# Kernel optimization log

Measured on AMD Instinct MI355X. Metric: run time of the kernel, lower is better.

Reference implementation:

```python
import jax, jax.numpy as jnp
import numpy as np

B, N, D = 8, 1024, 384
L, NH = 2, 8
HD = D // NH
HID2 = 4 * D  # project_in output channels = 2 * hidden = 2 * (2*dim) = 1536
HID = 2 * D  # GDFN hidden = 768


def setup_inputs() -> dict:
    key = jax.random.key(0)
    ks = jax.random.split(key, 16)
    s = 0.02
    return {
        "x": jax.random.normal(ks[0], (B, N, D), jnp.float32),
        "qkv_w": jax.random.normal(ks[1], (L, 3 * D, D), jnp.float32) * s,
        "qkv_b": jnp.zeros((L, 3 * D), jnp.float32),
        "proj_w": jax.random.normal(ks[2], (L, D, D), jnp.float32) * s,
        "proj_b": jnp.zeros((L, D), jnp.float32),
        "ln1_g": jnp.ones((L, D), jnp.float32),
        "ln1_b": jnp.zeros((L, D), jnp.float32),
        "ln2_g": jnp.ones((L, D), jnp.float32),
        "ln2_b": jnp.zeros((L, D), jnp.float32),
        "pin_w": jax.random.normal(ks[3], (L, HID2, D), jnp.float32) * s,
        "pin_b": jnp.zeros((L, HID2), jnp.float32),
        "dw_w": jax.random.normal(ks[4], (L, HID2, 1, 3, 3), jnp.float32) * s,
        "dw_b": jnp.zeros((L, HID2), jnp.float32),
        "pout_w": jax.random.normal(ks[5], (L, D, HID), jnp.float32) * s,
        "pout_b": jnp.zeros((L, D), jnp.float32),
    }


def _ln(y, g, b, eps=1e-5):
    m = y.mean(-1, keepdims=True)
    v = ((y - m) ** 2).mean(-1, keepdims=True)
    return (y - m) / jnp.sqrt(v + eps) * g + b


def _decay_bias(n, num_heads):
    # bias[h,i,j] = |i-j| * log(1 - 2^(-2 - 4*h/num_heads))  (negative)
    h = jnp.arange(num_heads, dtype=jnp.float32)
    decay = jnp.log(1.0 - 2.0 ** (-2.0 - 4.0 * h / num_heads))
    idx = jnp.arange(n, dtype=jnp.float32)
    dist = jnp.abs(idx[:, None] - idx[None, :])
    return dist[None] * decay[:, None, None]  # [NH, N, N]


def reference(x, qkv_w, qkv_b, proj_w, proj_b, ln1_g, ln1_b, ln2_g, ln2_b,
              pin_w, pin_b, dw_w, dw_b, pout_w, pout_b):
    b, n, d = x.shape
    hs = ws = int(np.sqrt(n))
    bias = _decay_bias(n, NH).astype(x.dtype)
    scale = HD ** -0.5
    nl = qkv_w.shape[0]
    for l in range(nl):
        # --- MHSA with spectral decay bias ---
        res = x
        xn = _ln(x, ln1_g[l], ln1_b[l])
        qkv = xn @ qkv_w[l].T + qkv_b[l]
        q, k, v = jnp.split(qkv, 3, axis=-1)
        q = q.reshape(b, n, NH, HD).transpose(0, 2, 1, 3)  # bhnd
        k = k.reshape(b, n, NH, HD).transpose(0, 2, 1, 3)
        v = v.reshape(b, n, NH, HD).transpose(0, 2, 1, 3)
        scores = jnp.einsum('bhnd,bhmd->bhnm', q, k) * scale + bias[None]
        attn = jax.nn.softmax(scores, axis=-1)
        out = jnp.einsum('bhnm,bhmd->bhnd', attn, v)
        out = out.transpose(0, 2, 1, 3).reshape(b, n, d)
        x = res + out @ proj_w[l].T + proj_b[l]
        # --- GDFN ---
        res = x
        xn = _ln(x, ln2_g[l], ln2_b[l])
        img = xn.transpose(0, 2, 1).reshape(b, d, hs, ws)  # NCHW
        h = jnp.einsum('oc,bchw->bohw', pin_w[l], img) + pin_b[l][None, :, None, None]
        h = jax.lax.conv_general_dilated(
            h, dw_w[l], window_strides=(1, 1), padding=[(1, 1), (1, 1)],
            feature_group_count=h.shape[1],
            dimension_numbers=('NCHW', 'OIHW', 'NCHW')) + dw_b[l][None, :, None, None]
        h1, h2 = jnp.split(h, 2, axis=1)
        g = jax.nn.gelu(h1, approximate=False) * h2
        o = jnp.einsum('oc,bchw->bohw', pout_w[l], g) + pout_b[l][None, :, None, None]
        x = res + o.reshape(b, d, n).transpose(0, 2, 1)
    return x
```

## Files before the change

kernel.cpp:

```cpp
#include <hip/hip_runtime.h>
#include <math.h>

#define B_ 8
#define N_ 1024
#define D_ 384
#define NH_ 8
#define HD_ 48
#define HID2_ 1536
#define HID_ 768
#define M_ (B_*N_)

typedef __attribute__((ext_vector_type(4))) float f32x4;
typedef __attribute__((ext_vector_type(2))) float f32x2;
typedef __attribute__((ext_vector_type(8))) short bf16x8;
typedef __attribute__((ext_vector_type(4))) short bf16x4;
typedef __attribute__((ext_vector_type(2))) unsigned u32x2;
typedef __attribute__((ext_vector_type(4))) unsigned u32x4;

__device__ inline unsigned short f2bf(float f) {
    unsigned u = __builtin_bit_cast(unsigned, f);
    u += 0x7fff + ((u >> 16) & 1);
    return (unsigned short)(u >> 16);
}
__device__ inline float bf2f(unsigned short h) {
    unsigned u = ((unsigned)h) << 16;
    return __builtin_bit_cast(float, u);
}
__device__ inline unsigned cvtpk_bf16(float lo, float hi) {
    unsigned r;
    asm("v_cvt_pk_bf16_f32 %0, %1, %2" : "=v"(r) : "v"(lo), "v"(hi));
    return r;
}
__device__ inline f32x4 mfma16(bf16x4 a, bf16x4 b, f32x4 c) {
#if __has_builtin(__builtin_amdgcn_mfma_f32_16x16x16bf16_1k)
    return __builtin_amdgcn_mfma_f32_16x16x16bf16_1k(a, b, c, 0, 0, 0);
#else
    asm("v_mfma_f32_16x16x16_bf16 %0, %1, %2, %0" : "+v"(c) : "v"(a), "v"(b));
    return c;
#endif
}

__global__ __launch_bounds__(256) void cvt4_kernel(
    const float* __restrict__ s1, const float* __restrict__ s2,
    const float* __restrict__ s3, const float* __restrict__ s4,
    int c1, int c2, int c3, int c4, unsigned short* __restrict__ out) {
    int i = blockIdx.x * 256 + threadIdx.x;
    if (i >= c1 + c2 + c3 + c4) return;
    const float* src; int off = i;
    if (i < c1) { src = s1; }
    else if (i < c1 + c2) { src = s2; off = i - c1; }
    else if (i < c1 + c2 + c3) { src = s3; off = i - c1 - c2; }
    else { src = s4; off = i - c1 - c2 - c3; }
    f32x4 v = *(const f32x4*)(src + (size_t)off*4);
    ushort4 o;
    o.x = f2bf(v[0]); o.y = f2bf(v[1]); o.z = f2bf(v[2]); o.w = f2bf(v[3]);
    *(ushort4*)(out + (size_t)i*4) = o;
}

__global__ __launch_bounds__(256) void ln_kernel(
    const float* __restrict__ x, const float* __restrict__ g,
    const float* __restrict__ b, unsigned short* __restrict__ out) {
    int wave = threadIdx.x >> 6;
    int lane = threadIdx.x & 63;
    int row  = blockIdx.x * 4 + wave;
    const float* xr = x + (size_t)row * D_;
    f32x2 v[3];
    float s = 0.f;
    #pragma unroll
    for (int i = 0; i < 3; ++i) {
        v[i] = *(const f32x2*)(xr + i*128 + lane*2);
        s += v[i][0] + v[i][1];
    }
    #pragma unroll
    for (int off = 1; off < 64; off <<= 1) s += __shfl_xor(s, off);
    float mean = s * (1.0f/D_);
    float vs = 0.f;
    #pragma unroll
    for (int i = 0; i < 3; ++i) {
        float t0 = v[i][0]-mean, t1 = v[i][1]-mean;
        vs += t0*t0 + t1*t1;
    }
    #pragma unroll
    for (int off = 1; off < 64; off <<= 1) vs += __shfl_xor(vs, off);
    float rstd = rsqrtf(vs * (1.0f/D_) + 1e-5f);
    unsigned short* orow = out + (size_t)row * D_;
    #pragma unroll
    for (int i = 0; i < 3; ++i) {
        int d = i*128 + lane*2;
        ushort2 o;
        o.x = f2bf((v[i][0]-mean)*rstd*g[d]   + b[d]);
        o.y = f2bf((v[i][1]-mean)*rstd*g[d+1] + b[d+1]);
        *(ushort2*)(orow + d) = o;
    }
}

template<int MODE>
__global__ __launch_bounds__(256) void gemm_bf16(
    const unsigned short* __restrict__ A, const unsigned short* __restrict__ W,
    const float* __restrict__ bias, const float* __restrict__ res,
    void* __restrict__ outv, int M, int O, int K) {
    __shared__ unsigned short a_s[128][40];
    __shared__ unsigned short w_s[128][40];
    int tid = threadIdx.x;
    int o0 = blockIdx.x * 128;
    int m0 = blockIdx.y * 128;
    int wave = tid >> 6, lane = tid & 63;
    int wm = wave >> 1, wn = wave & 1;
    int lr = lane & 15, lc = lane >> 4;
    int r0 = tid >> 2, ch = tid & 3;
    int r1 = r0 + 64;
    f32x4 acc[4][4];
    #pragma unroll
    for (int i=0;i<4;++i)
      #pragma unroll
      for (int j=0;j<4;++j) acc[i][j] = (f32x4){0.f,0.f,0.f,0.f};

    const unsigned short* pa0 = A + (size_t)(m0+r0)*K + ch*8;
    const unsigned short* pa1 = A + (size_t)(m0+r1)*K + ch*8;
    const unsigned short* pw0 = W + (size_t)(o0+r0)*K + ch*8;
    const unsigned short* pw1 = W + (size_t)(o0+r1)*K + ch*8;
    bf16x8 a0 = *(const bf16x8*)pa0, a1 = *(const bf16x8*)pa1;
    bf16x8 w0 = *(const bf16x8*)pw0, w1 = *(const bf16x8*)pw1;

    for (int k0 = 0; k0 < K; k0 += 32) {
        __syncthreads();
        *(bf16x8*)&a_s[r0][ch*8] = a0;
        *(bf16x8*)&a_s[r1][ch*8] = a1;
        *(bf16x8*)&w_s[r0][ch*8] = w0;
        *(bf16x8*)&w_s[r1][ch*8] = w1;
        __syncthreads();
        if (k0 + 32 < K) {
            pa0 += 32; pa1 += 32; pw0 += 32; pw1 += 32;
            a0 = *(const bf16x8*)pa0; a1 = *(const bf16x8*)pa1;
            w0 = *(const bf16x8*)pw0; w1 = *(const bf16x8*)pw1;
        }
        bf16x8 af[4], wf[4];
        #pragma unroll
        for (int i = 0; i < 4; ++i)
            af[i] = *(const bf16x8*)&a_s[wm*64 + i*16 + lr][lc*8];
        #pragma unroll
        for (int j = 0; j < 4; ++j)
            wf[j] = *(const bf16x8*)&w_s[wn*64 + j*16 + lr][lc*8];
        #pragma unroll
        for (int i = 0; i < 4; ++i)
            #pragma unroll
            for (int j = 0; j < 4; ++j)
                acc[i][j] = __builtin_amdgcn_mfma_f32_16x16x32_bf16(
                    af[i], wf[j], acc[i][j], 0, 0, 0);
    }
    #pragma unroll
    for (int i = 0; i < 4; ++i) {
        int mbase = m0 + wm*64 + i*16 + lc*4;
        #pragma unroll
        for (int j = 0; j < 4; ++j) {
            int oc = o0 + wn*64 + j*16 + lr;
            float bv = bias[oc];
            #pragma unroll
            for (int r = 0; r < 4; ++r) {
                int m = mbase + r;
                float v = acc[i][j][r] + bv;
                if (MODE == 1) {
                    ((float*)outv)[(size_t)m*O + oc] = v + res[(size_t)m*O + oc];
                } else {
                    ((unsigned short*)outv)[(size_t)m*O + oc] = f2bf(v);
                }
            }
        }
    }
}

template<int MODE>
__global__ __launch_bounds__(256) void gemm_bf16_s(
    const unsigned short* __restrict__ A, const unsigned short* __restrict__ W,
    const float* __restrict__ bias, const float* __restrict__ res,
    void* __restrict__ outv, int M, int O, int K) {
    __shared__ unsigned short a_s[64][72];
    __shared__ unsigned short w_s[64][72];
    int tid = threadIdx.x;
    int o0 = blockIdx.x * 64;
    int m0 = blockIdx.y * 64;
    int wave = tid >> 6, lane = tid & 63;
    int lr = lane & 15, lc = lane >> 4;
    int r = tid >> 2, c = (tid & 3) * 16;
    f32x4 acc[4];
    #pragma unroll
    for (int i=0;i<4;++i) acc[i] = (f32x4){0.f,0.f,0.f,0.f};

    const unsigned short* pa = A + (size_t)(m0+r)*K + c;
    const unsigned short* pw = W + (size_t)(o0+r)*K + c;
    bf16x8 a0 = *(const bf16x8*)pa, a1 = *(const bf16x8*)(pa+8);
    bf16x8 w0 = *(const bf16x8*)pw, w1 = *(const bf16x8*)(pw+8);

    for (int k0 = 0; k0 < K; k0 += 64) {
        __syncthreads();
        *(bf16x8*)&a_s[r][c]   = a0;
        *(bf16x8*)&a_s[r][c+8] = a1;
        *(bf16x8*)&w_s[r][c]   = w0;
        *(bf16x8*)&w_s[r][c+8] = w1;
        __syncthreads();
        if (k0 + 64 < K) {
            pa += 64; pw += 64;
            a0 = *(const bf16x8*)pa; a1 = *(const bf16x8*)(pa+8);
            w0 = *(const bf16x8*)pw; w1 = *(const bf16x8*)(pw+8);
        }
        #pragma unroll
        for (int ks = 0; ks < 2; ++ks) {
            bf16x8 wf = *(const bf16x8*)&w_s[wave*16 + lr][ks*32 + lc*8];
            #pragma unroll
            for (int i = 0; i < 4; ++i) {
                bf16x8 af = *(const bf16x8*)&a_s[i*16 + lr][ks*32 + lc*8];
                acc[i] = __builtin_amdgcn_mfma_f32_16x16x32_bf16(af, wf, acc[i], 0,0,0);
            }
        }
    }
    int oc = o0 + wave*16 + lr;
    float bv = bias[oc];
    #pragma unroll
    for (int i = 0; i < 4; ++i) {
        #pragma unroll
        for (int rr = 0; rr < 4; ++rr) {
            int m = m0 + i*16 + lc*4 + rr;
            float v = acc[i][rr] + bv;
            if (MODE == 1) {
                ((float*)outv)[(size_t)m*O + oc] = v + res[(size_t)m*O + oc];
            } else {
                ((unsigned short*)outv)[(size_t)m*O + oc] = f2bf(v);
            }
        }
    }
}

__global__ __launch_bounds__(256) void attn_mfma(
    const unsigned short* __restrict__ qkv, unsigned short* __restrict__ out) {
    __shared__ unsigned short k_s[64][72];
    __shared__ unsigned short vt_s[48][72];
    int tid = threadIdx.x;
    int wave = tid >> 6, lane = tid & 63;
    int lr = lane & 15, lc = lane >> 4;
    int b = blockIdx.x >> 3, h = blockIdx.x & 7;
    int q0 = blockIdx.y * 64;
    const float LOG2E = 1.4426950408889634f;
    float decay_nats = logf(1.0f - exp2f(-2.0f - 0.5f*(float)h));
    float decay = decay_nats * LOG2E;
    const float scale2 = 0.14433756729740643f * LOG2E;
    const bf16x8 zero8 = {0,0,0,0,0,0,0,0};

    int bandi = (int)(20.0f / (-decay_nats));
    int lo = q0 - bandi - 63;
    int kt_lo = lo > 0 ? (lo >> 6) : 0;
    int kt_hi = (q0 + 63 + bandi) >> 6;
    if (kt_hi > 15) kt_hi = 15;

    if (tid < 192) {
        int zr = tid / 3, zc = 48 + (tid % 3) * 8;
        *(bf16x8*)&k_s[zr][zc] = zero8;
    }

    int q = q0 + wave*16 + lr;
    float qqf = (float)q;
    const unsigned short* qrow = qkv + ((size_t)b*N_ + q)*1152 + h*48;
    bf16x8 qf0 = *(const bf16x8*)(qrow + lc*8);
    bf16x8 qf1 = zero8;
    if (lc < 2) qf1 = *(const bf16x8*)(qrow + 32 + lc*8);

    const unsigned short* kbase = qkv + (size_t)b*N_*1152 + D_ + h*48;
    int kr0 = tid / 6, kc0 = (tid % 6) * 8;
    bool kact1 = tid < 128;
    int s1 = kact1 ? tid + 256 : 0;
    int kr1 = s1 / 6, kc1 = (s1 % 6) * 8;
    const unsigned short* kp0 = kbase + (size_t)(kt_lo*64 + kr0)*1152 + kc0;
    const unsigned short* kp1 = kbase + (size_t)(kt_lo*64 + kr1)*1152 + kc1;

    int vd2 = (tid >> 3) * 2;
    int vch = tid & 7;
    bool vact = tid < 192;
    const unsigned short* vp = kbase + D_ + (size_t)(kt_lo*64 + vch*8)*1152 + vd2;

    float m_i = -3e38f, l_i = 0.f;
    f32x4 oacc[3];
    #pragma unroll
    for (int i=0;i<3;++i) oacc[i] = (f32x4){0.f,0.f,0.f,0.f};

    for (int kt = kt_lo; kt <= kt_hi; ++kt) {
        int n0 = kt * 64;
        bf16x8 kv0 = *(const bf16x8*)kp0;  kp0 += 64*1152;
        bf16x8 kv1 = zero8;
        if (kact1) kv1 = *(const bf16x8*)kp1;
        kp1 += 64*1152;
        unsigned vv[8];
        if (vact) {
            #pragma unroll
            for (int i = 0; i < 8; ++i)
                vv[i] = *(const unsigned*)(vp + (size_t)i*1152);
        }
        vp += 64*1152;
        __syncthreads();
        *(bf16x8*)&k_s[kr0][kc0] = kv0;
        if (kact1) *(bf16x8*)&k_s[kr1][kc1] = kv1;
        if (vact) {
            u32x4 wlo, whi;
            #pragma unroll
            for (int i = 0; i < 4; ++i) {
                wlo[i] = (vv[2*i] & 0xffffu) | (vv[2*i+1] << 16);
                whi[i] = (vv[2*i] >> 16)    | (vv[2*i+1] & 0xffff0000u);
            }
            *(bf16x8*)&vt_s[vd2]  [vch*8] = __builtin_bit_cast(bf16x8, wlo);
            *(bf16x8*)&vt_s[vd2+1][vch*8] = __builtin_bit_cast(bf16x8, whi);
        }
        __syncthreads();
        f32x4 sc[4];
        #pragma unroll
        for (int f = 0; f < 4; ++f) {
            sc[f] = (f32x4){0.f,0.f,0.f,0.f};
            bf16x8 kf0 = *(const bf16x8*)&k_s[f*16 + lr][lc*8];
            bf16x8 kf1 = *(const bf16x8*)&k_s[f*16 + lr][32 + lc*8];
            sc[f] = __builtin_amdgcn_mfma_f32_16x16x32_bf16(kf0, qf0, sc[f],0,0,0);
            sc[f] = __builtin_amdgcn_mfma_f32_16x16x32_bf16(kf1, qf1, sc[f],0,0,0);
        }
        float s2[4][4];
        float kv0f = (float)(n0 + lc*4);
        float mt = -3e38f;
        #pragma unroll
        for (int f = 0; f < 4; ++f)
            #pragma unroll
            for (int r = 0; r < 4; ++r) {
                float kk = kv0f + (float)(f*16 + r);
                s2[f][r] = sc[f][r]*scale2 + fabsf(qqf - kk)*decay;
                mt = fmaxf(mt, s2[f][r]);
            }
        mt = fmaxf(mt, __shfl_xor(mt, 16));
        mt = fmaxf(mt, __shfl_xor(mt, 32));
        float mn = fmaxf(m_i, mt);
        float alpha = __builtin_amdgcn_exp2f(m_i - mn);
        m_i = mn;
        l_i *= alpha;
        #pragma unroll
        for (int md = 0; md < 3; ++md)
            #pragma unroll
            for (int r = 0; r < 4; ++r) oacc[md][r] *= alpha;
        float ps = 0.f;
        #pragma unroll
        for (int f = 0; f < 4; ++f)
            #pragma unroll
            for (int r = 0; r < 4; ++r) {
                s2[f][r] = __builtin_amdgcn_exp2f(s2[f][r] - m_i);
                ps += s2[f][r];
            }
        ps += __shfl_xor(ps, 16);
        ps += __shfl_xor(ps, 32);
        l_i += ps;
        bf16x4 pfrag[4];
        #pragma unroll
        for (int f = 0; f < 4; ++f) {
            u32x2 u;
            u[0] = cvtpk_bf16(s2[f][0], s2[f][1]);
            u[1] = cvtpk_bf16(s2[f][2], s2[f][3]);
            pfrag[f] = __builtin_bit_cast(bf16x4, u);
        }
        #pragma unroll
        for (int f = 0; f < 4; ++f)
            #pragma unroll
            for (int md = 0; md < 3; ++md) {
                bf16x4 va = *(const bf16x4*)&vt_s[md*16 + lr][f*16 + lc*4];
                oacc[md] = mfma16(va, pfrag[f], oacc[md]);
            }
    }
    float inv_l = 1.0f / l_i;
    #pragma unroll
    for (int md = 0; md < 3; ++md) {
        ushort4 o;
        o.x = f2bf(oacc[md][0]*inv_l);
        o.y = f2bf(oacc[md][1]*inv_l);
        o.z = f2bf(oacc[md][2]*inv_l);
        o.w = f2bf(oacc[md][3]*inv_l);
        *(ushort4*)(out + ((size_t)b*N_ + q)*D_ + h*48 + md*16 + lc*4) = o;
    }
}

__global__ __launch_bounds__(256) void dwconv_gate_bf16(
    const unsigned short* __restrict__ h, const float* __restrict__ dw_w,
    const float* __restrict__ dw_b, unsigned short* __restrict__ g) {
    __shared__ float wt_s[9][128];
    __shared__ float bs_s[128];
    int tid = threadIdx.x;
    int cg0 = blockIdx.x * 64;
    int y   = blockIdx.y;
    int b   = blockIdx.z;
    for (int i = tid; i < 1152; i += 256) {
        int tap = i >> 7, cl = i & 127;
        int gch = (cl < 64) ? (cg0 + cl) : (HID_ + cg0 + (cl - 64));
        wt_s[tap][cl] = dw_w[(size_t)gch*9 + tap];
    }
    if (tid < 128) {
        int gch = (tid < 64) ? (cg0 + tid) : (HID_ + cg0 + (tid - 64));
        bs_s[tid] = dw_b[gch];
    }
    __syncthreads();
    int x  = tid >> 3;
    int co = (tid & 7) * 8;
    int c1 = cg0 + co;
    const unsigned short* hb = h + (size_t)b*N_*HID2_;
    float acc1[8], acc2[8];
    #pragma unroll
    for (int j=0;j<8;++j) { acc1[j] = bs_s[co+j]; acc2[j] = bs_s[64+co+j]; }
    #pragma unroll
    for (int ky=0; ky<3; ++ky) {
        int yy = y + ky - 1;
        if (yy < 0 || yy >= 32) continue;
        #pragma unroll
        for (int kx=0; kx<3; ++kx) {
            int xx = x + kx - 1;
            if (xx < 0 || xx >= 32) continue;
            const unsigned short* p = hb + (size_t)(yy*32+xx)*HID2_ + c1;
            bf16x8 d1 = *(const bf16x8*)p;
            bf16x8 d2 = *(const bf16x8*)(p + HID_);
            int t = ky*3 + kx;
            f32x4 w1a = *(const f32x4*)&wt_s[t][co];
            f32x4 w1b = *(const f32x4*)&wt_s[t][co+4];
            f32x4 w2a = *(const f32x4*)&wt_s[t][64+co];
            f32x4 w2b = *(const f32x4*)&wt_s[t][64+co+4];
            #pragma unroll
            for (int j=0;j<4;++j) {
                acc1[j]   += bf2f((unsigned short)d1[j])   * w1a[j];
                acc1[j+4] += bf2f((unsigned short)d1[j+4]) * w1b[j];
                acc2[j]   += bf2f((unsigned short)d2[j])   * w2a[j];
                acc2[j+4] += bf2f((unsigned short)d2[j+4]) * w2b[j];
            }
        }
    }
    bf16x8 o;
    #pragma unroll
    for (int j=0;j<8;++j) {
        float ge = 0.5f*acc1[j]*(1.0f + erff(acc1[j]*0.70710678118f));
        o[j] = (short)f2bf(ge * acc2[j]);
    }
    *(bf16x8*)(g + (size_t)(b*N_ + y*32 + x)*HID_ + c1) = o;
}

extern "C" void kernel_launch(void* const* d_in, const int* in_sizes, int n_in,
                              void* d_out, int out_size, void* d_ws, size_t ws_size,
                              hipStream_t stream) {
    const float* x_in   = (const float*)d_in[0];
    const float* qkv_w  = (const float*)d_in[1];
    const float* qkv_b  = (const float*)d_in[2];
    const float* proj_w = (const float*)d_in[3];
    const float* proj_b = (const float*)d_in[4];
    const float* ln1_g  = (const float*)d_in[5];
    const float* ln1_b  = (const float*)d_in[6];
    const float* ln2_g  = (const float*)d_in[7];
    const float* ln2_b  = (const float*)d_in[8];
    const float* pin_w  = (const float*)d_in[9];
    const float* pin_b  = (const float*)d_in[10];
    const float* dw_w   = (const float*)d_in[11];
    const float* dw_b   = (const float*)d_in[12];
    const float* pout_w = (const float*)d_in[13];
    const float* pout_b = (const float*)d_in[14];

    float* pX = (float*)d_out;
    unsigned short* wXn  = (unsigned short*)d_ws;
    unsigned short* wQKV = wXn  + (size_t)M_*D_;
    unsigned short* wAO  = wQKV + (size_t)M_*3*D_;
    unsigned short* wH   = wAO  + (size_t)M_*D_;
    unsigned short* wG   = wH   + (size_t)M_*HID2_;
    unsigned short* wWq  = wG   + (size_t)M_*HID_;
    unsigned short* wWp  = wWq  + (size_t)2*3*D_*D_;
    unsigned short* wWi  = wWp  + (size_t)2*D_*D_;
    unsigned short* wWo  = wWi  + (size_t)2*HID2_*D_;

    int c1 = 2*3*D_*D_/4, c2 = 2*D_*D_/4, c3 = 2*HID2_*D_/4, c4 = 2*D_*HID_/4;
    int ctot = c1 + c2 + c3 + c4;
    cvt4_kernel<<<(ctot+255)/256, 256, 0, stream>>>(
        qkv_w, proj_w, pin_w, pout_w, c1, c2, c3, c4, wWq);

    hipMemcpyAsync(pX, x_in, sizeof(float)*(size_t)M_*D_,
                   hipMemcpyDeviceToDevice, stream);

    for (int l = 0; l < 2; ++l) {
        ln_kernel<<<M_/4, 256, 0, stream>>>(pX, ln1_g + l*D_, ln1_b + l*D_, wXn);
        gemm_bf16<0><<<dim3((3*D_)/128, M_/128), 256, 0, stream>>>(
            wXn, wWq + (size_t)l*3*D_*D_, qkv_b + (size_t)l*3*D_,
            nullptr, wQKV, M_, 3*D_, D_);
        attn_mfma<<<dim3(B_*NH_, N_/64), 256, 0, stream>>>(wQKV, wAO);
        gemm_bf16_s<1><<<dim3(D_/64, M_/64), 256, 0, stream>>>(
            wAO, wWp + (size_t)l*D_*D_, proj_b + (size_t)l*D_,
            pX, pX, M_, D_, D_);
        ln_kernel<<<M_/4, 256, 0, stream>>>(pX, ln2_g + l*D_, ln2_b + l*D_, wXn);
        gemm_bf16<0><<<dim3(HID2_/128, M_/128), 256, 0, stream>>>(
            wXn, wWi + (size_t)l*HID2_*D_, pin_b + (size_t)l*HID2_,
            nullptr, wH, M_, HID2_, D_);
        dwconv_gate_bf16<<<dim3(HID_/64, 32, B_), 256, 0, stream>>>(
            wH, dw_w + (size_t)l*HID2_*9, dw_b + (size_t)l*HID2_, wG);
        gemm_bf16_s<1><<<dim3(D_/64, M_/64), 256, 0, stream>>>(
            wG, wWo + (size_t)l*D_*HID_, pout_b + (size_t)l*D_,
            pX, pX, M_, D_, HID_);
    }
}
```

Baseline: 294.9 us.

## Split attention over key tiles with a separate log-sum-exp combine kernel

Splits each query block's banded key range into four chunks handled by separate blocks along a new grid dimension. Each writes unnormalized bf16 partial outputs plus running max and sum. A new combine kernel rescales and merges them. This aims to raise parallelism and balance load across heads with different band widths, at the cost of extra global traffic, an extra launch, and repeated Q loads. Partials reuse the GDFN workspace buffers.

Measured after the change: 308.8 us. 1.05x slower.

```diff
diff --git a/kernel.cpp b/kernel.cpp
--- a/kernel.cpp
+++ b/kernel.cpp
@@ -9,6 +9,7 @@
 #define HID2_ 1536
 #define HID_ 768
 #define M_ (B_*N_)
+#define NSPLIT 4
 
 typedef __attribute__((ext_vector_type(4))) float f32x4;
 typedef __attribute__((ext_vector_type(2))) float f32x2;
@@ -231,14 +232,17 @@
 }
 
 __global__ __launch_bounds__(256) void attn_mfma(
-    const unsigned short* __restrict__ qkv, unsigned short* __restrict__ out) {
+    const unsigned short* __restrict__ qkv,
+    unsigned short* __restrict__ o_part, float* __restrict__ ml_part) {
     __shared__ unsigned short k_s[64][72];
     __shared__ unsigned short vt_s[48][72];
     int tid = threadIdx.x;
     int wave = tid >> 6, lane = tid & 63;
     int lr = lane & 15, lc = lane >> 4;
-    int b = blockIdx.x >> 3, h = blockIdx.x & 7;
+    int bh = blockIdx.x;
+    int b = bh >> 3, h = bh & 7;
     int q0 = blockIdx.y * 64;
+    int sp = blockIdx.z;
     const float LOG2E = 1.4426950408889634f;
     float decay_nats = logf(1.0f - exp2f(-2.0f - 0.5f*(float)h));
     float decay = decay_nats * LOG2E;
@@ -250,6 +254,11 @@
     int kt_lo = lo > 0 ? (lo >> 6) : 0;
     int kt_hi = (q0 + 63 + bandi) >> 6;
     if (kt_hi > 15) kt_hi = 15;
+    int nt = kt_hi - kt_lo + 1;
+    int chunk = (nt + NSPLIT - 1) / NSPLIT;
+    int my_lo = kt_lo + sp * chunk;
+    int my_hi = my_lo + chunk - 1;
+    if (my_hi > kt_hi) my_hi = kt_hi;
 
     if (tid < 192) {
         int zr = tid / 3, zc = 48 + (tid % 3) * 8;
@@ -268,20 +277,20 @@
     bool kact1 = tid < 128;
     int s1 = kact1 ? tid + 256 : 0;
     int kr1 = s1 / 6, kc1 = (s1 % 6) * 8;
-    const unsigned short* kp0 = kbase + (size_t)(kt_lo*64 + kr0)*1152 + kc0;
-    const unsigned short* kp1 = kbase + (size_t)(kt_lo*64 + kr1)*1152 + kc1;
+    const unsigned short* kp0 = kbase + (size_t)(my_lo*64 + kr0)*1152 + kc0;
+    const unsigned short* kp1 = kbase + (size_t)(my_lo*64 + kr1)*1152 + kc1;
 
     int vd2 = (tid >> 3) * 2;
     int vch = tid & 7;
     bool vact = tid < 192;
-    const unsigned short* vp = kbase + D_ + (size_t)(kt_lo*64 + vch*8)*1152 + vd2;
+    const unsigned short* vp = kbase + D_ + (size_t)(my_lo*64 + vch*8)*1152 + vd2;
 
     float m_i = -3e38f, l_i = 0.f;
     f32x4 oacc[3];
     #pragma unroll
     for (int i=0;i<3;++i) oacc[i] = (f32x4){0.f,0.f,0.f,0.f};
 
-    for (int kt = kt_lo; kt <= kt_hi; ++kt) {
+    for (int kt = my_lo; kt <= my_hi; ++kt) {
         int n0 = kt * 64;
         bf16x8 kv0 = *(const bf16x8*)kp0;  kp0 += 64*1152;
         bf16x8 kv1 = zero8;
@@ -365,16 +374,54 @@
                 oacc[md] = mfma16(va, pfrag[f], oacc[md]);
             }
     }
-    float inv_l = 1.0f / l_i;
+    size_t pq = ((size_t)sp*64 + bh)*1024 + q;
     #pragma unroll
     for (int md = 0; md < 3; ++md) {
-        ushort4 o;
-        o.x = f2bf(oacc[md][0]*inv_l);
-        o.y = f2bf(oacc[md][1]*inv_l);
-        o.z = f2bf(oacc[md][2]*inv_l);
-        o.w = f2bf(oacc[md][3]*inv_l);
-        *(ushort4*)(out + ((size_t)b*N_ + q)*D_ + h*48 + md*16 + lc*4) = o;
-    }
+        u32x2 u;
+        u[0] = cvtpk_bf16(oacc[md][0], oacc[md][1]);
+        u[1] = cvtpk_bf16(oacc[md][2], oacc[md][3]);
+        *(u32x2*)(o_part + pq*48 + md*16 + lc*4) = u;
+    }
+    if (lc == 0) {
+        f32x2 ml; ml[0] = m_i; ml[1] = l_i;
+        *(f32x2*)(ml_part + pq*2) = ml;
+    }
+}
+
+__global__ __launch_bounds__(256) void attn_combine(
+    const unsigned short* __restrict__ o_part, const float* __restrict__ ml_part,
+    unsigned short* __restrict__ out) {
+    int idx = blockIdx.x * 256 + threadIdx.x;
+    int d4 = (idx % 12) * 4;
+    int q  = (idx / 12) & 1023;
+    int bh = idx / (12*1024);
+    int b = bh >> 3, h = bh & 7;
+    float m[NSPLIT], l[NSPLIT];
+    #pragma unroll
+    for (int s = 0; s < NSPLIT; ++s) {
+        const float* ml = ml_part + (((size_t)s*64 + bh)*1024 + q)*2;
+        m[s] = ml[0]; l[s] = ml[1];
+    }
+    float mx = m[0];
+    #pragma unroll
+    for (int s = 1; s < NSPLIT; ++s) mx = fmaxf(mx, m[s]);
+    f32x4 num = {0.f,0.f,0.f,0.f};
+    float den = 0.f;
+    #pragma unroll
+    for (int s = 0; s < NSPLIT; ++s) {
+        float w = __builtin_amdgcn_exp2f(m[s] - mx);
+        den += w * l[s];
+        bf16x4 ov = *(const bf16x4*)(o_part +
+            ((((size_t)s*64 + bh)*1024 + q)*48 + d4));
+        #pragma unroll
+        for (int j = 0; j < 4; ++j)
+            num[j] += w * bf2f((unsigned short)ov[j]);
+    }
+    float inv = 1.0f / den;
+    ushort4 o;
+    o.x = f2bf(num[0]*inv); o.y = f2bf(num[1]*inv);
+    o.z = f2bf(num[2]*inv); o.w = f2bf(num[3]*inv);
+    *(ushort4*)(out + ((size_t)b*N_ + q)*D_ + h*48 + d4) = o;
 }
 
 __global__ __launch_bounds__(256) void dwconv_gate_bf16(
@@ -467,6 +514,9 @@
     unsigned short* wWi  = wWp  + (size_t)2*D_*D_;
     unsigned short* wWo  = wWi  + (size_t)2*HID2_*D_;
 
+    unsigned short* oPart = wH;
+    float* mlPart = (float*)wG;
+
     int c1 = 2*3*D_*D_/4, c2 = 2*D_*D_/4, c3 = 2*HID2_*D_/4, c4 = 2*D_*HID_/4;
     int ctot = c1 + c2 + c3 + c4;
     cvt4_kernel<<<(ctot+255)/256, 256, 0, stream>>>(
@@ -480,7 +530,10 @@
         gemm_bf16<0><<<dim3((3*D_)/128, M_/128), 256, 0, stream>>>(
             wXn, wWq + (size_t)l*3*D_*D_, qkv_b + (size_t)l*3*D_,
             nullptr, wQKV, M_, 3*D_, D_);
-        attn_mfma<<<dim3(B_*NH_, N_/64), 256, 0, stream>>>(wQKV, wAO);
+        attn_mfma<<<dim3(B_*NH_, N_/64, NSPLIT), 256, 0, stream>>>(
+            wQKV, oPart, mlPart);
+        attn_combine<<<(B_*NH_*N_*12)/256, 256, 0, stream>>>(
+            oPart, mlPart, wAO);
         gemm_bf16_s<1><<<dim3(D_/64, M_/64), 256, 0, stream>>>(
             wAO, wWp + (size_t)l*D_*D_, proj_b + (size_t)l*D_,
             pX, pX, M_, D_, D_);
```

## Double-buffer K/V shared tiles and prefetch next tile into registers in attention

Applied to the files above, without the earlier changes.

The attention kernel now keeps two shared-memory buffers for the K and transposed-V tiles. Global loads for the next key tile are issued into registers right after the barrier, so they overlap with the current tile's MFMA and softmax work. This removes one __syncthreads per iteration and hides global load latency. In exchange it doubles the LDS footprint and raises register pressure, which could lower occupancy.

After: 289.6 us. About the same (-1.8%).

```diff
diff --git a/kernel.cpp b/kernel.cpp
--- a/kernel.cpp
+++ b/kernel.cpp
@@ -232,8 +232,8 @@
 
 __global__ __launch_bounds__(256) void attn_mfma(
     const unsigned short* __restrict__ qkv, unsigned short* __restrict__ out) {
-    __shared__ unsigned short k_s[64][72];
-    __shared__ unsigned short vt_s[48][72];
+    __shared__ unsigned short k_s[2][64][72];
+    __shared__ unsigned short vt_s[2][48][72];
     int tid = threadIdx.x;
     int wave = tid >> 6, lane = tid & 63;
     int lr = lane & 15, lc = lane >> 4;
@@ -253,7 +253,8 @@
 
     if (tid < 192) {
         int zr = tid / 3, zc = 48 + (tid % 3) * 8;
-        *(bf16x8*)&k_s[zr][zc] = zero8;
+        *(bf16x8*)&k_s[0][zr][zc] = zero8;
+        *(bf16x8*)&k_s[1][zr][zc] = zero8;
     }
 
     int q = q0 + wave*16 + lr;
@@ -276,44 +277,56 @@
     bool vact = tid < 192;
     const unsigned short* vp = kbase + D_ + (size_t)(kt_lo*64 + vch*8)*1152 + vd2;
 
+    bf16x8 rk0 = *(const bf16x8*)kp0;  kp0 += 64*1152;
+    bf16x8 rk1 = zero8;
+    if (kact1) rk1 = *(const bf16x8*)kp1;
+    kp1 += 64*1152;
+    unsigned rv[8];
+    if (vact) {
+        #pragma unroll
+        for (int i = 0; i < 8; ++i)
+            rv[i] = *(const unsigned*)(vp + (size_t)i*1152);
+    }
+    vp += 64*1152;
+
     float m_i = -3e38f, l_i = 0.f;
     f32x4 oacc[3];
     #pragma unroll
     for (int i=0;i<3;++i) oacc[i] = (f32x4){0.f,0.f,0.f,0.f};
 
+    int cur = 0;
     for (int kt = kt_lo; kt <= kt_hi; ++kt) {
         int n0 = kt * 64;
-        bf16x8 kv0 = *(const bf16x8*)kp0;  kp0 += 64*1152;
-        bf16x8 kv1 = zero8;
-        if (kact1) kv1 = *(const bf16x8*)kp1;
-        kp1 += 64*1152;
-        unsigned vv[8];
-        if (vact) {
-            #pragma unroll
-            for (int i = 0; i < 8; ++i)
-                vv[i] = *(const unsigned*)(vp + (size_t)i*1152);
-        }
-        vp += 64*1152;
-        __syncthreads();
-        *(bf16x8*)&k_s[kr0][kc0] = kv0;
-        if (kact1) *(bf16x8*)&k_s[kr1][kc1] = kv1;
+        *(bf16x8*)&k_s[cur][kr0][kc0] = rk0;
+        if (kact1) *(bf16x8*)&k_s[cur][kr1][kc1] = rk1;
         if (vact) {
             u32x4 wlo, whi;
             #pragma unroll
             for (int i = 0; i < 4; ++i) {
-                wlo[i] = (vv[2*i] & 0xffffu) | (vv[2*i+1] << 16);
-                whi[i] = (vv[2*i] >> 16)    | (vv[2*i+1] & 0xffff0000u);
-            }
-            *(bf16x8*)&vt_s[vd2]  [vch*8] = __builtin_bit_cast(bf16x8, wlo);
-            *(bf16x8*)&vt_s[vd2+1][vch*8] = __builtin_bit_cast(bf16x8, whi);
+                wlo[i] = (rv[2*i] & 0xffffu) | (rv[2*i+1] << 16);
+                whi[i] = (rv[2*i] >> 16)    | (rv[2*i+1] & 0xffff0000u);
+            }
+            *(bf16x8*)&vt_s[cur][vd2]  [vch*8] = __builtin_bit_cast(bf16x8, wlo);
+            *(bf16x8*)&vt_s[cur][vd2+1][vch*8] = __builtin_bit_cast(bf16x8, whi);
         }
         __syncthreads();
+        if (kt < kt_hi) {
+            rk0 = *(const bf16x8*)kp0;  kp0 += 64*1152;
+            if (kact1) rk1 = *(const bf16x8*)kp1;
+            kp1 += 64*1152;
+            if (vact) {
+                #pragma unroll
+                for (int i = 0; i < 8; ++i)
+                    rv[i] = *(const unsigned*)(vp + (size_t)i*1152);
+            }
+            vp += 64*1152;
+        }
         f32x4 sc[4];
         #pragma unroll
         for (int f = 0; f < 4; ++f) {
             sc[f] = (f32x4){0.f,0.f,0.f,0.f};
-            bf16x8 kf0 = *(const bf16x8*)&k_s[f*16 + lr][lc*8];
-            bf16x8 kf1 = *(const bf16x8*)&k_s[f*16 + lr][32 + lc*8];
+            bf16x8 kf0 = *(const bf16x8*)&k_s[cur][f*16 + lr][lc*8];
+            bf16x8 kf1 = *(const bf16x8*)&k_s[cur][f*16 + lr][32 + lc*8];
             sc[f] = __builtin_amdgcn_mfma_f32_16x16x32_bf16(kf0, qf0, sc[f],0,0,0);
             sc[f] = __builtin_amdgcn_mfma_f32_16x16x32_bf16(kf1, qf1, sc[f],0,0,0);
         }
@@ -361,9 +374,10 @@
         for (int f = 0; f < 4; ++f)
             #pragma unroll
             for (int md = 0; md < 3; ++md) {
-                bf16x4 va = *(const bf16x4*)&vt_s[md*16 + lr][f*16 + lc*4];
+                bf16x4 va = *(const bf16x4*)&vt_s[cur][md*16 + lr][f*16 + lc*4];
                 oacc[md] = mfma16(va, pfrag[f], oacc[md]);
             }
+        cur ^= 1;
     }
     float inv_l = 1.0f / l_i;
     #pragma unroll
```
